# Performance work log

Measured on AMD Instinct MI355X. Metric: run time of the kernel, lower is better.

The kernel has to match this reference:

```python
import jax, jax.numpy as jnp
import numpy as np

N_NODES = 50000
N_EDGES = 800000
HIDDEN = 128
HEADS = 4
LAYERS = 2
NEG_SLOPE = 0.2


def setup_inputs() -> dict:
    key = jax.random.key(0)
    ks = jax.random.split(key, 12)
    s_in = 1.0 / np.sqrt(HIDDEN)
    x = jax.random.normal(ks[0], (N_NODES, HIDDEN), dtype=jnp.float32)
    edge_index = jax.random.randint(ks[1], (2, N_EDGES), 0, N_NODES, dtype=jnp.int64)
    conv_w = jax.random.normal(ks[2], (LAYERS, HIDDEN, HEADS * HIDDEN), dtype=jnp.float32) * s_in
    att_src = jax.random.normal(ks[3], (LAYERS, HEADS, HIDDEN), dtype=jnp.float32) * s_in
    att_dst = jax.random.normal(ks[4], (LAYERS, HEADS, HIDDEN), dtype=jnp.float32) * s_in
    conv_b = jax.random.normal(ks[5], (LAYERS, HIDDEN), dtype=jnp.float32) * 0.01
    proj_w = jax.random.normal(ks[6], (LAYERS, HIDDEN, HIDDEN), dtype=jnp.float32) * s_in
    proj_b = jax.random.normal(ks[7], (LAYERS, HIDDEN), dtype=jnp.float32) * 0.01
    skip_w = jax.random.normal(ks[8], (LAYERS, HIDDEN, HIDDEN), dtype=jnp.float32) * s_in
    skip_b = jax.random.normal(ks[9], (LAYERS, HIDDEN), dtype=jnp.float32) * 0.01
    return {"x": x, "edge_index": edge_index, "conv_w": conv_w, "att_src": att_src,
            "att_dst": att_dst, "conv_b": conv_b, "proj_w": proj_w, "proj_b": proj_b,
            "skip_w": skip_w, "skip_b": skip_b}


def _gat_layer(x, src, dst, W, a_s, a_d, b):
    # x: [N, D]; W: [D, H*C]; a_s, a_d: [H, C]; b: [C]
    N = x.shape[0]
    h = (x @ W).reshape(N, HEADS, HIDDEN)          # [N, H, C]
    alpha_src = jnp.einsum('nhc,hc->nh', h, a_s)   # [N, H]
    alpha_dst = jnp.einsum('nhc,hc->nh', h, a_d)   # [N, H]
    alpha = alpha_src[src] + alpha_dst[dst]        # [E, H]
    alpha = jnp.where(alpha >= 0, alpha, NEG_SLOPE * alpha)  # leaky_relu(0.2)
    amax = jax.ops.segment_max(alpha, dst, num_segments=N)   # [N, H]
    ex = jnp.exp(alpha - amax[dst])                # [E, H]
    denom = jax.ops.segment_sum(ex, dst, num_segments=N)     # [N, H]
    w = ex / (denom[dst] + 1e-16)                  # PyG softmax eps
    msg = h[src] * w[:, :, None]                   # [E, H, C]
    out = jax.ops.segment_sum(msg, dst, num_segments=N)      # [N, H, C]
    return out.mean(axis=1) + b                    # concat=False -> head mean


def reference(x, edge_index, conv_w, att_src, att_dst, conv_b, proj_w, proj_b, skip_w, skip_b):
    src, dst = edge_index[0], edge_index[1]
    out = x
    for l in range(LAYERS):
        conv = _gat_layer(out, src, dst, conv_w[l], att_src[l], att_dst[l], conv_b[l])
        out = jax.nn.relu(conv) @ proj_w[l] + proj_b[l] + (out @ skip_w[l] + skip_b[l])
    return out
```

## Files before the change

### kernel.cpp

```cpp
#include <hip/hip_runtime.h>
#include <hip/hip_bf16.h>
#include <stdint.h>

#define N_NODES 50000
#define N_EDGES 800000
#define HIDDEN  128
#define HEADS   4
#define HD      (HEADS*HIDDEN)
#define CAST_Q  (N_NODES*HIDDEN/4)
#define NTILES  (N_NODES/16)

typedef __attribute__((ext_vector_type(8))) short  short8;
typedef __attribute__((ext_vector_type(4))) float  floatx4;
typedef __attribute__((ext_vector_type(2))) float  floatx2;

static __device__ __forceinline__ unsigned short bf16_bits(float f) {
    __hip_bfloat16 h = __float2bfloat16(f);
    union { __hip_bfloat16 b; unsigned short s; } u; u.b = h; return u.s;
}

static __device__ __forceinline__ float lexp(float a) {
    return __expf(fmaxf(a, 0.2f * a));
}


#if __has_builtin(__builtin_amdgcn_cvt_pk_fp8_f32) && __has_builtin(__builtin_amdgcn_cvt_pk_f32_fp8)
#define FP8_HW 1
#else
#define FP8_HW 0
static __device__ __forceinline__ unsigned fp8_enc1(float f) {
    unsigned s = __float_as_uint(f) >> 31;
    float a = fabsf(f);
    if (a < 0.0009765625f) return s << 7;
    if (a > 448.f) a = 448.f;
    unsigned ub = __float_as_uint(a) + 0x00080000u;
    int e = (int)((ub >> 23) & 255) - 120;
    unsigned m = (ub >> 20) & 7;
    if (e <= 0) {
        int mm = (int)(a * 512.f + 0.5f); if (mm > 7) mm = 7;
        return (s << 7) | (unsigned)mm;
    }
    if (e > 15) { e = 15; m = 7; }
    return (s << 7) | ((unsigned)e << 3) | m;
}
static __device__ __forceinline__ floatx2 fp8_dec_pk(unsigned b2) {
    floatx2 r;
    unsigned b = b2 & 255;
    {
        unsigned s = (b >> 7) & 1, e = (b >> 3) & 15, m = b & 7;
        r.x = (e == 0) ? ((s ? -1.f : 1.f) * (float)m * 0.001953125f)
                       : __uint_as_float((s << 31) | ((e + 120) << 23) | (m << 20));
    }
    b = (b2 >> 8) & 255;
    {
        unsigned s = (b >> 7) & 1, e = (b >> 3) & 15, m = b & 7;
        r.y = (e == 0) ? ((s ? -1.f : 1.f) * (float)m * 0.001953125f)
                       : __uint_as_float((s << 31) | ((e + 120) << 23) | (m << 20));
    }
    return r;
}
#endif

static __device__ __forceinline__ unsigned fp8_pack4(float a, float b, float c, float d) {
#if FP8_HW
    int w = __builtin_amdgcn_cvt_pk_fp8_f32(a, b, 0, false);
    w     = __builtin_amdgcn_cvt_pk_fp8_f32(c, d, w, true);
    return (unsigned)w;
#else
    return fp8_enc1(a) | (fp8_enc1(b) << 8) | (fp8_enc1(c) << 16) | (fp8_enc1(d) << 24);
#endif
}

static __device__ __forceinline__ void accf8p(floatx2* acc2, uint2 u, float wt) {
    floatx2 wv = {wt, wt};
#if FP8_HW
    acc2[0] += wv * __builtin_amdgcn_cvt_pk_f32_fp8((int)u.x, false);
    acc2[1] += wv * __builtin_amdgcn_cvt_pk_f32_fp8((int)u.x, true);
    acc2[2] += wv * __builtin_amdgcn_cvt_pk_f32_fp8((int)u.y, false);
    acc2[3] += wv * __builtin_amdgcn_cvt_pk_f32_fp8((int)u.y, true);
#else
    acc2[0] += wv * fp8_dec_pk(u.x);
    acc2[1] += wv * fp8_dec_pk(u.x >> 16);
    acc2[2] += wv * fp8_dec_pk(u.y);
    acc2[3] += wv * fp8_dec_pk(u.y >> 16);
#endif
}


__global__ __launch_bounds__(256) void prep_k(
        const float* __restrict__ x, unsigned short* __restrict__ xb16,
        const float* __restrict__ conv_w, const float* __restrict__ proj_w,
        const float* __restrict__ skip_w,
        unsigned short* __restrict__ cwb, unsigned short* __restrict__ pwb,
        unsigned short* __restrict__ swb,
        const int* __restrict__ dst, int* __restrict__ cnt) {
    int i = blockIdx.x * 256 + threadIdx.x;
    if (i < CAST_Q) {
        float4 v = ((const float4*)x)[i];
        uint2 p;
        p.x = (unsigned)bf16_bits(v.x) | ((unsigned)bf16_bits(v.y) << 16);
        p.y = (unsigned)bf16_bits(v.z) | ((unsigned)bf16_bits(v.w) << 16);
        ((uint2*)xb16)[i] = p;
        return;
    }
    int o = i - CAST_Q;
    if (o >= 196608) {
        int e = o - 196608;
        if (e < N_EDGES) atomicAdd(&cnt[dst[e]], 1);
        return;
    }
    const float* B; unsigned short* D; int off, N; bool perm = false;
    if (o < 131072)      { B = conv_w + (o >> 16) * 65536; D = cwb + (o >> 16) * 65536; off = o & 65535; N = 512; }
    else if (o < 163840) { int t = o - 131072; B = proj_w + (t >> 14) * 16384; D = pwb + (t >> 14) * 16384; off = t & 16383; N = 128; perm = true; }
    else                 { int t = o - 163840; B = skip_w + (t >> 14) * 16384; D = swb + (t >> 14) * 16384; off = t & 16383; N = 128; }
    int j = off & 7, r = (off >> 3) & 15, q = (off >> 7) & 3;
    int rest = off >> 9, ntn = N >> 4;
    int nt = rest % ntn, kc = rest / ntn;
    int kr = kc * 32 + q * 8 + j;
    int row = perm ? ((kr & 7) * 16 + (kr >> 3)) : kr;
    D[off] = bf16_bits(B[(size_t)row * N + nt * 16 + r]);
}


__global__ __launch_bounds__(1024) void scan1_k(int* __restrict__ cnt,
                                                int* __restrict__ bsum, int n) {
    __shared__ int buf[1024];
    int t = threadIdx.x, i = blockIdx.x * 1024 + t;
    int v = (i < n) ? cnt[i] : 0;
    buf[t] = v;
    __syncthreads();
    for (int off = 1; off < 1024; off <<= 1) {
        int xv = (t >= off) ? buf[t - off] : 0;
        __syncthreads();
        buf[t] += xv;
        __syncthreads();
    }
    if (i < n) cnt[i] = buf[t] - v;
    if (t == 1023) bsum[blockIdx.x] = buf[1023];
}

__global__ void scan2_k(int* __restrict__ bsum, int nb) {
    if (threadIdx.x == 0) {
        int acc = 0;
        for (int i = 0; i < nb; ++i) { int v = bsum[i]; bsum[i] = acc; acc += v; }
    }
}

__global__ __launch_bounds__(256) void scansc_k(const int* __restrict__ src,
                                                const int* __restrict__ dst,
                                                const int* __restrict__ cnt,
                                                const int* __restrict__ bsum,
                                                int* __restrict__ fill,
                                                int* __restrict__ src_sorted,
                                                int* __restrict__ row_ptr) {
    int i = blockIdx.x * 256 + threadIdx.x;
    if (i < N_EDGES) {
        int d = dst[i];
        int p = cnt[d] + bsum[d >> 10] + atomicAdd(&fill[d], 1);
        src_sorted[p] = src[i];
        return;
    }
    int j = i - N_EDGES;
    if (j < N_NODES) {
        row_ptr[j] = cnt[j] + bsum[j >> 10];
        if (j == 0) row_ptr[N_NODES] = N_EDGES;
    }
}


__global__ __launch_bounds__(256, 2) void gemmc_k(
        const __hip_bfloat16* __restrict__ A,
        const unsigned short* __restrict__ Bs,
        const float* __restrict__ att_s, const float* __restrict__ att_d,
        unsigned char* __restrict__ h8,
        float* __restrict__ a_src, float* __restrict__ a_dst, int mtiles) {
    int head = threadIdx.x >> 6;
    int lane = threadIdx.x & 63;
    int r = lane & 15, q = lane >> 4;

    short8 Bf[4][8];
#pragma unroll
    for (int kc = 0; kc < 4; ++kc)
#pragma unroll
        for (int ntl = 0; ntl < 8; ++ntl)
            Bf[kc][ntl] = *(const short8*)((const short*)Bs +
                (((size_t)(kc * 32 + head * 8 + ntl) * 4 + q) * 128 + r * 8));

    float as_r[8], ad_r[8];
#pragma unroll
    for (int ntl = 0; ntl < 8; ++ntl) {
        as_r[ntl] = att_s[head * HIDDEN + ntl * 16 + r];
        ad_r[ntl] = att_d[head * HIDDEN + ntl * 16 + r];
    }

    const int stride = gridDim.x;
    int mt = blockIdx.x;
    short8 av[4];
    if (mt < mtiles) {
        const short* Ab = (const short*)A + (size_t)(mt * 16 + r) * HIDDEN + q * 8;
#pragma unroll
        for (int kc = 0; kc < 4; ++kc) av[kc] = *(const short8*)(Ab + kc * 32);
    }
    while (mt < mtiles) {
        int nmt = mt + stride;
        short8 avn[4];
        if (nmt < mtiles) {
            const short* Ab = (const short*)A + (size_t)(nmt * 16 + r) * HIDDEN + q * 8;
#pragma unroll
            for (int kc = 0; kc < 4; ++kc) avn[kc] = *(const short8*)(Ab + kc * 32);
        }
        int m0 = mt * 16;
        floatx4 acc[8];
#pragma unroll
        for (int i = 0; i < 8; ++i) acc[i] = (floatx4){0.f, 0.f, 0.f, 0.f};
#pragma unroll
        for (int kc = 0; kc < 4; ++kc)
#pragma unroll
            for (int ntl = 0; ntl < 8; ++ntl)
                acc[ntl] = __builtin_amdgcn_mfma_f32_16x16x32_bf16(av[kc], Bf[kc][ntl], acc[ntl], 0, 0, 0);

#pragma unroll
        for (int i = 0; i < 4; ++i) {
            uint2 o;
            o.x = fp8_pack4(acc[0][i], acc[1][i], acc[2][i], acc[3][i]);
            o.y = fp8_pack4(acc[4][i], acc[5][i], acc[6][i], acc[7][i]);
            *(uint2*)(h8 + (size_t)(m0 + q * 4 + i) * HD + head * HIDDEN + r * 8) = o;
        }
        float sA[4] = {0, 0, 0, 0}, sD[4] = {0, 0, 0, 0};
#pragma unroll
        for (int ntl = 0; ntl < 8; ++ntl)
#pragma unroll
            for (int i = 0; i < 4; ++i) {
                sA[i] += acc[ntl][i] * as_r[ntl];
                sD[i] += acc[ntl][i] * ad_r[ntl];
            }
#pragma unroll
        for (int d = 1; d < 16; d <<= 1)
#pragma unroll
            for (int i = 0; i < 4; ++i) {
                sA[i] += __shfl_xor(sA[i], d);
                sD[i] += __shfl_xor(sD[i], d);
            }
        if (r == 0)
#pragma unroll
            for (int i = 0; i < 4; ++i) {
                int row = m0 + q * 4 + i;
                a_src[row * HEADS + head] = sA[i];
                a_dst[row * HEADS + head] = sD[i];
            }
        mt = nmt;
#pragma unroll
        for (int kc = 0; kc < 4; ++kc) av[kc] = avn[kc];
    }
}


template <typename OutT>
__global__ __launch_bounds__(256, 2) void gemmp_k(
        const __hip_bfloat16* __restrict__ A,  const unsigned short* __restrict__ Bs,
        const __hip_bfloat16* __restrict__ A2, const unsigned short* __restrict__ Bs2,
        const float* __restrict__ b1, const float* __restrict__ b2,
        OutT* __restrict__ D, int mtiles) {
    int wave = threadIdx.x >> 6;
    int lane = threadIdx.x & 63;
    int r = lane & 15, q = lane >> 4;
    int nh = wave & 1;

    short8 Bf[4][4], Bf2[4][4];
#pragma unroll
    for (int kc = 0; kc < 4; ++kc)
#pragma unroll
        for (int ntl = 0; ntl < 4; ++ntl) {
            size_t off = (((size_t)(kc * 8 + nh * 4 + ntl) * 4 + q) * 128 + r * 8);
            Bf[kc][ntl]  = *(const short8*)((const short*)Bs  + off);
            Bf2[kc][ntl] = *(const short8*)((const short*)Bs2 + off);
        }
    float bias[4];
#pragma unroll
    for (int ntl = 0; ntl < 4; ++ntl) {
        int col = nh * 64 + ntl * 16 + r;
        bias[ntl] = b1[col] + b2[col];
    }

    const int stride = gridDim.x * 2;
    int mt = blockIdx.x * 2 + (wave >> 1);
    short8 av[4], av2[4];
    if (mt < mtiles) {
        const short* Ab  = (const short*)A  + (size_t)(mt * 16 + r) * HIDDEN + q * 8;
        const short* Ab2 = (const short*)A2 + (size_t)(mt * 16 + r) * HIDDEN + q * 8;
#pragma unroll
        for (int kc = 0; kc < 4; ++kc) {
            av[kc]  = *(const short8*)(Ab  + kc * 32);
            av2[kc] = *(const short8*)(Ab2 + kc * 32);
        }
    }
    while (mt < mtiles) {
        int nmt = mt + stride;
        short8 avn[4], avn2[4];
        if (nmt < mtiles) {
            const short* Ab  = (const short*)A  + (size_t)(nmt * 16 + r) * HIDDEN + q * 8;
            const short* Ab2 = (const short*)A2 + (size_t)(nmt * 16 + r) * HIDDEN + q * 8;
#pragma unroll
            for (int kc = 0; kc < 4; ++kc) {
                avn[kc]  = *(const short8*)(Ab  + kc * 32);
                avn2[kc] = *(const short8*)(Ab2 + kc * 32);
            }
        }
        int m0 = mt * 16;
        floatx4 acc[4];
#pragma unroll
        for (int i = 0; i < 4; ++i) acc[i] = (floatx4){0.f, 0.f, 0.f, 0.f};
#pragma unroll
        for (int kc = 0; kc < 4; ++kc)
#pragma unroll
            for (int ntl = 0; ntl < 4; ++ntl) {
                acc[ntl] = __builtin_amdgcn_mfma_f32_16x16x32_bf16(av[kc],  Bf[kc][ntl],  acc[ntl], 0, 0, 0);
                acc[ntl] = __builtin_amdgcn_mfma_f32_16x16x32_bf16(av2[kc], Bf2[kc][ntl], acc[ntl], 0, 0, 0);
            }
#pragma unroll
        for (int ntl = 0; ntl < 4; ++ntl) {
            int col = nh * 64 + ntl * 16 + r;
#pragma unroll
            for (int i = 0; i < 4; ++i) {
                int row = m0 + q * 4 + i;
                float v = acc[ntl][i] + bias[ntl];
                if constexpr (sizeof(OutT) == 4)
                    ((float*)D)[(size_t)row * HIDDEN + col] = v;
                else
                    ((__hip_bfloat16*)D)[(size_t)row * HIDDEN + col] = __float2bfloat16(v);
            }
        }
        mt = nmt;
#pragma unroll
        for (int kc = 0; kc < 4; ++kc) { av[kc] = avn[kc]; av2[kc] = avn2[kc]; }
    }
}


__global__ __launch_bounds__(256) void msg_k(const int* __restrict__ row_ptr,
                                             const int* __restrict__ src_sorted,
                                             const float* __restrict__ a_src,
                                             const float* __restrict__ a_dst,
                                             const unsigned char* __restrict__ h8,
                                             const float* __restrict__ conv_b,
                                             __hip_bfloat16* __restrict__ rc) {
    int wave = threadIdx.x >> 6;
    int lane = threadIdx.x & 63;
    int n = blockIdx.x * 4 + wave;
    if (n >= N_NODES) return;
    int head = lane >> 4;
    float adn = a_dst[n * HEADS + head];
    int beg = row_ptr[n], end = row_ptr[n + 1];
    const uint2* hq = (const uint2*)h8;

    floatx2 acc2[4];
#pragma unroll
    for (int k = 0; k < 4; ++k) acc2[k] = (floatx2){0.f, 0.f};
    float esum = 0.f;
    for (int base = beg; base < end; base += 32) {
        int m = min(32, end - base);
        int sv = (lane < m) ? src_sorted[base + lane] : 0;
        int j = 0;
        for (; j + 4 <= m; j += 4) {
            int s0 = __shfl(sv, j),     s1 = __shfl(sv, j + 1);
            int s2 = __shfl(sv, j + 2), s3 = __shfl(sv, j + 3);
            uint2 u0 = hq[(size_t)s0 * 64 + lane];
            uint2 u1 = hq[(size_t)s1 * 64 + lane];
            uint2 u2 = hq[(size_t)s2 * 64 + lane];
            uint2 u3 = hq[(size_t)s3 * 64 + lane];
            float e0 = lexp(a_src[s0 * 4 + head] + adn);
            float e1 = lexp(a_src[s1 * 4 + head] + adn);
            float e2 = lexp(a_src[s2 * 4 + head] + adn);
            float e3 = lexp(a_src[s3 * 4 + head] + adn);
            accf8p(acc2, u0, e0);
            accf8p(acc2, u1, e1);
            accf8p(acc2, u2, e2);
            accf8p(acc2, u3, e3);
            esum += (e0 + e1) + (e2 + e3);
        }
        for (; j < m; ++j) {
            int s0 = __shfl(sv, j);
            uint2 u0 = hq[(size_t)s0 * 64 + lane];
            float e0 = lexp(a_src[s0 * 4 + head] + adn);
            accf8p(acc2, u0, e0);
            esum += e0;
        }
    }
    float rinv = 1.f / (esum + 1e-16f);
    float acc[8];
#pragma unroll
    for (int k = 0; k < 4; ++k) { acc[2 * k] = acc2[k].x * rinv; acc[2 * k + 1] = acc2[k].y * rinv; }
#pragma unroll
    for (int k = 0; k < 8; ++k) {
        acc[k] += __shfl_xor(acc[k], 16);
        acc[k] += __shfl_xor(acc[k], 32);
    }
    if (lane < 16) {
        union { uint4 v; unsigned short us[8]; } o;
#pragma unroll
        for (int k = 0; k < 8; ++k) {
            float mres = 0.25f * acc[k] + conv_b[k * 16 + lane];
            o.us[k] = bf16_bits(mres > 0.f ? mres : 0.f);
        }
        ((uint4*)rc)[(size_t)n * 16 + lane] = o.v;
    }
}


extern "C" void kernel_launch(void* const* d_in, const int* in_sizes, int n_in,
                              void* d_out, int out_size, void* d_ws, size_t ws_size,
                              hipStream_t stream) {
    const float* x      = (const float*)d_in[0];
    const int*   ei     = (const int*)d_in[1];
    const float* conv_w = (const float*)d_in[2];
    const float* att_s  = (const float*)d_in[3];
    const float* att_d  = (const float*)d_in[4];
    const float* conv_b = (const float*)d_in[5];
    const float* proj_w = (const float*)d_in[6];
    const float* proj_b = (const float*)d_in[7];
    const float* skip_w = (const float*)d_in[8];
    const float* skip_b = (const float*)d_in[9];
    float* out = (float*)d_out;

    char* ws = (char*)d_ws;
    size_t o = 0;
    auto alloc = [&](size_t b) { size_t c = o; o += (b + 255) & ~(size_t)255; return c; };
    __hip_bfloat16* xb16 = (__hip_bfloat16*)(ws + alloc((size_t)N_NODES * HIDDEN * 2));
    unsigned short* cwb  = (unsigned short*)(ws + alloc((size_t)2 * HIDDEN * HD * 2));
    unsigned short* pwb  = (unsigned short*)(ws + alloc((size_t)2 * HIDDEN * HIDDEN * 2));
    unsigned short* swb  = (unsigned short*)(ws + alloc((size_t)2 * HIDDEN * HIDDEN * 2));
    unsigned char* h8    = (unsigned char*)(ws + alloc((size_t)N_NODES * HD));
    float* a_src         = (float*)(ws + alloc((size_t)N_NODES * HEADS * 4));
    float* a_dst         = (float*)(ws + alloc((size_t)N_NODES * HEADS * 4));
    int* row_ptr         = (int*)(ws + alloc((size_t)(N_NODES + 1) * 4));
    int* cntfill         = (int*)(ws + alloc((size_t)2 * N_NODES * 4));
    int* cnt  = cntfill;
    int* fill = cntfill + N_NODES;
    int* src_s           = (int*)(ws + alloc((size_t)N_EDGES * 4));
    __hip_bfloat16* rc   = (__hip_bfloat16*)(ws + alloc((size_t)N_NODES * HIDDEN * 2));
    __hip_bfloat16* xb   = (__hip_bfloat16*)(ws + alloc((size_t)N_NODES * HIDDEN * 2));
    int* bsum            = (int*)(ws + alloc(64 * 4));

    const int* srcp = ei;
    const int* dstp = ei + N_EDGES;

    (void)hipMemsetAsync(cntfill, 0, (size_t)2 * N_NODES * 4, stream);

    prep_k<<<(CAST_Q + 196608 + N_EDGES + 255) / 256, 256, 0, stream>>>(
        x, (unsigned short*)xb16, conv_w, proj_w, skip_w, cwb, pwb, swb, dstp, cnt);

    const int nb = (N_NODES + 1023) / 1024;
    scan1_k<<<nb, 1024, 0, stream>>>(cnt, bsum, N_NODES);
    scan2_k<<<1, 64, 0, stream>>>(bsum, nb);
    scansc_k<<<(N_EDGES + N_NODES + 255) / 256, 256, 0, stream>>>(
        srcp, dstp, cnt, bsum, fill, src_s, row_ptr);

    const __hip_bfloat16* xc = xb16;
    for (int l = 0; l < 2; ++l) {
        gemmc_k<<<512, 256, 0, stream>>>(
            xc, cwb + (size_t)l * HIDDEN * HD,
            att_s + l * HD, att_d + l * HD, h8, a_src, a_dst, NTILES);
        msg_k<<<(N_NODES + 3) / 4, 256, 0, stream>>>(
            row_ptr, src_s, a_src, a_dst, h8, conv_b + l * HIDDEN, rc);
        if (l == 0)
            gemmp_k<__hip_bfloat16><<<512, 256, 0, stream>>>(
                rc, pwb + (size_t)l * HIDDEN * HIDDEN,
                xc, swb + (size_t)l * HIDDEN * HIDDEN,
                proj_b + l * HIDDEN, skip_b + l * HIDDEN, xb, NTILES);
        else
            gemmp_k<float><<<512, 256, 0, stream>>>(
                rc, pwb + (size_t)l * HIDDEN * HIDDEN,
                xc, swb + (size_t)l * HIDDEN * HIDDEN,
                proj_b + l * HIDDEN, skip_b + l * HIDDEN, out, NTILES);
        xc = xb;
    }
}
```

Measured before the change: 355.2 us.

## Replace global-atomic CSR build with two-pass bucketed counting sort

Builds the destination-sorted edge list with a two-level counting sort instead of per-node global atomics. Edges are first histogrammed into 196 coarse buckets per 8192-edge tile in shared memory, scanned in one block, and scattered into a temp buffer that reuses the rc workspace. Each bucket is then sorted by its low 8 bits in shared memory, which also writes row_ptr. This removes the memset and the contended global atomics on 50k counters, at the cost of packing src into 16 bits (valid only because node ids stay below 65536) and a single-block scan.

```diff
diff --git a/kernel.cpp b/kernel.cpp
--- a/kernel.cpp
+++ b/kernel.cpp
@@ -9,6 +9,13 @@
 #define HD      (HEADS*HIDDEN)
 #define CAST_Q  (N_NODES*HIDDEN/4)
 #define NTILES  (N_NODES/16)
+
+#define NBUCK   196
+#define TILE_H  8192
+#define NBLK_H  ((N_EDGES + TILE_H - 1) / TILE_H)
+#define NBH     (NBUCK * NBLK_H)
+#define SWZ_N   196608
+#define HIST_B0 ((CAST_Q + SWZ_N) / 256)
 
 typedef __attribute__((ext_vector_type(8))) short  short8;
 typedef __attribute__((ext_vector_type(4))) float  floatx4;
@@ -93,7 +100,22 @@
         const float* __restrict__ skip_w,
         unsigned short* __restrict__ cwb, unsigned short* __restrict__ pwb,
         unsigned short* __restrict__ swb,
-        const int* __restrict__ dst, int* __restrict__ cnt) {
+        const int* __restrict__ dst, int* __restrict__ bh) {
+    __shared__ int hh[NBUCK];
+    if (blockIdx.x >= HIST_B0) {
+        int blk = blockIdx.x - HIST_B0;
+        for (int c = threadIdx.x; c < NBUCK; c += 256) hh[c] = 0;
+        __syncthreads();
+        int e0 = blk * TILE_H;
+#pragma unroll
+        for (int i = 0; i < TILE_H / 256; ++i) {
+            int e = e0 + threadIdx.x + i * 256;
+            if (e < N_EDGES) atomicAdd(&hh[dst[e] >> 8], 1);
+        }
+        __syncthreads();
+        for (int c = threadIdx.x; c < NBUCK; c += 256) bh[c * NBLK_H + blk] = hh[c];
+        return;
+    }
     int i = blockIdx.x * 256 + threadIdx.x;
     if (i < CAST_Q) {
         float4 v = ((const float4*)x)[i];
@@ -104,11 +126,6 @@
         return;
     }
     int o = i - CAST_Q;
-    if (o >= 196608) {
-        int e = o - 196608;
-        if (e < N_EDGES) atomicAdd(&cnt[dst[e]], 1);
-        return;
-    }
     const float* B; unsigned short* D; int off, N; bool perm = false;
     if (o < 131072)      { B = conv_w + (o >> 16) * 65536; D = cwb + (o >> 16) * 65536; off = o & 65535; N = 512; }
     else if (o < 163840) { int t = o - 131072; B = proj_w + (t >> 14) * 16384; D = pwb + (t >> 14) * 16384; off = t & 16383; N = 128; perm = true; }
@@ -122,12 +139,21 @@
 }
 
 
-__global__ __launch_bounds__(1024) void scan1_k(int* __restrict__ cnt,
-                                                int* __restrict__ bsum, int n) {
+#define SCAN_PT ((NBH + 1023) / 1024)
+
+__global__ __launch_bounds__(1024) void scanA_k(int* __restrict__ bh) {
     __shared__ int buf[1024];
-    int t = threadIdx.x, i = blockIdx.x * 1024 + t;
-    int v = (i < n) ? cnt[i] : 0;
-    buf[t] = v;
+    int t = threadIdx.x;
+    int base = t * SCAN_PT;
+    int loc[SCAN_PT];
+    int s = 0;
+#pragma unroll
+    for (int i = 0; i < SCAN_PT; ++i) {
+        int idx = base + i;
+        int v = (idx < NBH) ? bh[idx] : 0;
+        loc[i] = s; s += v;
+    }
+    buf[t] = s;
     __syncthreads();
     for (int off = 1; off < 1024; off <<= 1) {
         int xv = (t >= off) ? buf[t - off] : 0;
@@ -135,35 +161,67 @@
         buf[t] += xv;
         __syncthreads();
     }
-    if (i < n) cnt[i] = buf[t] - v;
-    if (t == 1023) bsum[blockIdx.x] = buf[1023];
-}
-
-__global__ void scan2_k(int* __restrict__ bsum, int nb) {
-    if (threadIdx.x == 0) {
-        int acc = 0;
-        for (int i = 0; i < nb; ++i) { int v = bsum[i]; bsum[i] = acc; acc += v; }
-    }
-}
-
-__global__ __launch_bounds__(256) void scansc_k(const int* __restrict__ src,
-                                                const int* __restrict__ dst,
-                                                const int* __restrict__ cnt,
-                                                const int* __restrict__ bsum,
-                                                int* __restrict__ fill,
-                                                int* __restrict__ src_sorted,
-                                                int* __restrict__ row_ptr) {
-    int i = blockIdx.x * 256 + threadIdx.x;
-    if (i < N_EDGES) {
-        int d = dst[i];
-        int p = cnt[d] + bsum[d >> 10] + atomicAdd(&fill[d], 1);
-        src_sorted[p] = src[i];
-        return;
-    }
-    int j = i - N_EDGES;
-    if (j < N_NODES) {
-        row_ptr[j] = cnt[j] + bsum[j >> 10];
-        if (j == 0) row_ptr[N_NODES] = N_EDGES;
+    int excl = buf[t] - s;
+#pragma unroll
+    for (int i = 0; i < SCAN_PT; ++i) {
+        int idx = base + i;
+        if (idx < NBH) bh[idx] = excl + loc[i];
+    }
+}
+
+
+__global__ __launch_bounds__(256) void scatterA_k(const int* __restrict__ src,
+                                                  const int* __restrict__ dst,
+                                                  const int* __restrict__ bh,
+                                                  unsigned* __restrict__ tmp) {
+    __shared__ int cnt[NBUCK];
+    int t = threadIdx.x, blk = blockIdx.x;
+    for (int c = t; c < NBUCK; c += 256) cnt[c] = bh[c * NBLK_H + blk];
+    __syncthreads();
+    int e0 = blk * TILE_H;
+#pragma unroll
+    for (int i = 0; i < TILE_H / 256; ++i) {
+        int e = e0 + t + i * 256;
+        if (e < N_EDGES) {
+            int d = dst[e];
+            int pos = atomicAdd(&cnt[d >> 8], 1);
+            tmp[pos] = ((unsigned)(d & 255) << 16) | (unsigned)src[e];
+        }
+    }
+}
+
+
+__global__ __launch_bounds__(256) void sortB_k(const unsigned* __restrict__ tmp,
+                                               const int* __restrict__ bh,
+                                               int* __restrict__ src_sorted,
+                                               int* __restrict__ row_ptr) {
+    __shared__ int cnt[256], buf[256], pos[256];
+    int t = threadIdx.x, b = blockIdx.x;
+    int beg = bh[b * NBLK_H];
+    int end = (b == NBUCK - 1) ? N_EDGES : bh[(b + 1) * NBLK_H];
+    cnt[t] = 0;
+    __syncthreads();
+    for (int i = beg + t; i < end; i += 256) atomicAdd(&cnt[(tmp[i] >> 16) & 255], 1);
+    __syncthreads();
+    int v = cnt[t];
+    buf[t] = v;
+    __syncthreads();
+    for (int off = 1; off < 256; off <<= 1) {
+        int xv = (t >= off) ? buf[t - off] : 0;
+        __syncthreads();
+        buf[t] += xv;
+        __syncthreads();
+    }
+    int excl = buf[t] - v;
+    int d = b * 256 + t;
+    if (d <= N_NODES) row_ptr[d] = beg + excl;
+    pos[t] = excl;
+    __syncthreads();
+    for (int i = beg + t; i < end; i += 256) {
+        unsigned w = tmp[i];
+        int c = (w >> 16) & 255;
+        int p = beg + atomicAdd(&pos[c], 1);
+        src_sorted[p] = (int)(w & 0xFFFFu);
     }
 }
 
@@ -433,27 +491,21 @@
     float* a_src         = (float*)(ws + alloc((size_t)N_NODES * HEADS * 4));
     float* a_dst         = (float*)(ws + alloc((size_t)N_NODES * HEADS * 4));
     int* row_ptr         = (int*)(ws + alloc((size_t)(N_NODES + 1) * 4));
-    int* cntfill         = (int*)(ws + alloc((size_t)2 * N_NODES * 4));
-    int* cnt  = cntfill;
-    int* fill = cntfill + N_NODES;
     int* src_s           = (int*)(ws + alloc((size_t)N_EDGES * 4));
     __hip_bfloat16* rc   = (__hip_bfloat16*)(ws + alloc((size_t)N_NODES * HIDDEN * 2));
     __hip_bfloat16* xb   = (__hip_bfloat16*)(ws + alloc((size_t)N_NODES * HIDDEN * 2));
-    int* bsum            = (int*)(ws + alloc(64 * 4));
+    int* bh              = (int*)(ws + alloc((size_t)NBH * 4));
+
+    unsigned* tmp = (unsigned*)rc;
 
     const int* srcp = ei;
     const int* dstp = ei + N_EDGES;
 
-    (void)hipMemsetAsync(cntfill, 0, (size_t)2 * N_NODES * 4, stream);
-
-    prep_k<<<(CAST_Q + 196608 + N_EDGES + 255) / 256, 256, 0, stream>>>(
-        x, (unsigned short*)xb16, conv_w, proj_w, skip_w, cwb, pwb, swb, dstp, cnt);
-
-    const int nb = (N_NODES + 1023) / 1024;
-    scan1_k<<<nb, 1024, 0, stream>>>(cnt, bsum, N_NODES);
-    scan2_k<<<1, 64, 0, stream>>>(bsum, nb);
-    scansc_k<<<(N_EDGES + N_NODES + 255) / 256, 256, 0, stream>>>(
-        srcp, dstp, cnt, bsum, fill, src_s, row_ptr);
+    prep_k<<<HIST_B0 + NBLK_H, 256, 0, stream>>>(
+        x, (unsigned short*)xb16, conv_w, proj_w, skip_w, cwb, pwb, swb, dstp, bh);
+    scanA_k<<<1, 1024, 0, stream>>>(bh);
+    scatterA_k<<<NBLK_H, 256, 0, stream>>>(srcp, dstp, bh, tmp);
+    sortB_k<<<NBUCK, 256, 0, stream>>>(tmp, bh, src_s, row_ptr);
 
     const __hip_bfloat16* xc = xb16;
     for (int l = 0; l < 2; ++l) {
```

Measured after the change: 331.2 us. -6.7%, faster.
